# Kernel optimization log

Hardware: AMD Instinct MI355X
Metric: run time of the kernel (lower is better)

The kernel has to match this reference:

```python
import jax, jax.numpy as jnp
import numpy as np

H = 128
B, N = 8, 200
EPS = 1e-5


def _linear(v, W, b):
    return v @ W.T + b


def _masked_bn(v, m, gamma, beta):
    # v: (..., H); m: (...,) float 0/1 mask. BatchNorm1d over masked rows only
    # (track_running_stats=False -> batch statistics, biased variance).
    mf = m[..., None]
    axes = tuple(range(v.ndim - 1))
    cnt = jnp.maximum(jnp.sum(m), 1.0)
    mean = jnp.sum(v * mf, axis=axes) / cnt            # (H,)
    var = jnp.sum(mf * (v - mean) ** 2, axis=axes) / cnt
    vn = (v - mean) * jax.lax.rsqrt(var + EPS) * gamma + beta
    return jnp.where(mf > 0, vn, v)


def setup_inputs() -> dict:
    key = jax.random.key(0)
    ks = jax.random.split(key, 16)
    s = 1.0 / np.sqrt(H)
    p = lambda k, shp: jax.random.uniform(k, shp, jnp.float32, -s, s)
    return {
        "x": jax.random.normal(ks[0], (B, N, H), jnp.float32),
        "e": jax.random.normal(ks[1], (B, N, N, H), jnp.float32),
        "mask": jax.random.randint(ks[2], (B, N), 0, 2, jnp.int32),
        "Ue_W": p(ks[3], (H, H)), "Ue_b": p(ks[4], (H,)),
        "Ve_W": p(ks[5], (H, H)), "Ve_b": p(ks[6], (H,)),
        "Un_W": p(ks[7], (H, H)), "Un_b": p(ks[8], (H,)),
        "Vn_W": p(ks[9], (H, H)), "Vn_b": p(ks[10], (H,)),
        "bn_n_g": jnp.ones((H,), jnp.float32), "bn_n_b": jnp.zeros((H,), jnp.float32),
        "bn_e_g": jnp.ones((H,), jnp.float32), "bn_e_b": jnp.zeros((H,), jnp.float32),
    }


def reference(x, e, mask, Ue_W, Ue_b, Ve_W, Ve_b, Un_W, Un_b, Vn_W, Vn_b,
              bn_n_g, bn_n_b, bn_e_g, bn_e_b):
    m = mask.astype(x.dtype)                      # (B,N)
    m1 = m[..., None]                             # (B,N,1)
    sq_mask = m[:, :, None] * m[:, None, :]       # (B,N,N)

    # EdgeFeatures: e_ij = U*e_ij + V*x_i + V*x_j (with node-masked Vx)
    Vx = m1 * _linear(x, Ve_W, Ve_b)              # (B,N,H)
    e_tmp = _linear(e, Ue_W, Ue_b) + Vx[:, :, None, :] + Vx[:, None, :, :]

    gate = jax.nn.sigmoid(e_tmp)                  # (B,N,N,H)
    gate_m = gate * sq_mask[..., None]            # mask rows and cols

    # NodeFeatures, sum aggregation: x_i = U*x_i + sum_j gate_ij * (V*x_j)
    Ux = m1 * _linear(x, Un_W, Un_b)
    Vxn = m1 * _linear(x, Vn_W, Vn_b)
    agg = jnp.einsum("bijh,bjh->bih", gate_m, Vxn)
    x_tmp = Ux + agg

    e_bn = _masked_bn(e_tmp, sq_mask, bn_e_g, bn_e_b)
    x_bn = _masked_bn(x_tmp, m, bn_n_g, bn_n_b)

    x_new = x + jax.nn.relu(x_bn)
    e_new = e + jax.nn.relu(e_bn)
    return x_new, e_new
```

## Files before the change

kernel.cpp:

```cpp
#include <hip/hip_runtime.h>
#include <hip/hip_bf16.h>

namespace {

typedef __attribute__((ext_vector_type(8))) short short8;
typedef __attribute__((ext_vector_type(4))) float f32x4;

constexpr int H = 128;
constexpr int N = 200;
constexpr int BN = 1600;
constexpr int X_SIZE = BN * H;
constexpr int NH = N * H;
constexpr int NT = 13;

constexpr int WS_VX    = 0;
constexpr int WS_UX    = WS_VX + X_SIZE;
constexpr int WS_VXN   = WS_UX + X_SIZE;
constexpr int WS_XTMP  = WS_VXN + X_SIZE;
constexpr int WS_ESUMS = WS_XTMP + X_SIZE;
constexpr int WS_ESSQS = WS_ESUMS + 32 * H;
constexpr int WS_NSUMS = WS_ESSQS + 32 * H;
constexpr int WS_NSSQS = WS_NSUMS + 32 * H;
constexpr int WS_STAT_END = WS_NSSQS + 32 * H;
constexpr int WS_ESC   = WS_STAT_END;
constexpr int WS_ESH   = WS_ESC + H;
constexpr int WS_NSC   = WS_ESH + H;
constexpr int WS_NSH   = WS_NSC + H;

__device__ __forceinline__ unsigned short f2bf(float f) {
  __hip_bfloat16 h = __float2bfloat16(f);
  return __builtin_bit_cast(unsigned short, h);
}

__device__ __forceinline__ short8 pack8(f32x4 a, f32x4 b) {
  short8 r;
  r[0] = (short)f2bf(a[0]); r[1] = (short)f2bf(a[1]);
  r[2] = (short)f2bf(a[2]); r[3] = (short)f2bf(a[3]);
  r[4] = (short)f2bf(b[0]); r[5] = (short)f2bf(b[1]);
  r[6] = (short)f2bf(b[2]); r[7] = (short)f2bf(b[3]);
  return r;
}

__device__ __forceinline__ int xcd_bi(int bid) {
  return (bid & 7) * N + (bid >> 3);
}

__global__ __launch_bounds__(128) void k_prep(
    const float* __restrict__ x, const int* __restrict__ mask,
    const float* __restrict__ VeW, const float* __restrict__ Veb,
    const float* __restrict__ UnW, const float* __restrict__ Unb,
    const float* __restrict__ VnW, const float* __restrict__ Vnb,
    float* __restrict__ ws) {
  const int bi = blockIdx.x, h = threadIdx.x;
  __shared__ float xr[H];
  xr[h] = x[bi * H + h];
  __syncthreads();
  const float mi = (float)mask[bi];
  float a0 = 0.f, a1 = 0.f, a2 = 0.f;
  #pragma unroll 4
  for (int k = 0; k < H; k += 4) {
    const float x0 = xr[k], x1 = xr[k + 1], x2 = xr[k + 2], x3 = xr[k + 3];
    float4 w;
    w = *(const float4*)&VeW[h * H + k];
    a0 += w.x * x0 + w.y * x1 + w.z * x2 + w.w * x3;
    w = *(const float4*)&UnW[h * H + k];
    a1 += w.x * x0 + w.y * x1 + w.z * x2 + w.w * x3;
    w = *(const float4*)&VnW[h * H + k];
    a2 += w.x * x0 + w.y * x1 + w.z * x2 + w.w * x3;
  }
  ws[WS_VX  + bi * H + h] = mi * (a0 + Veb[h]);
  ws[WS_UX  + bi * H + h] = mi * (a1 + Unb[h]);
  ws[WS_VXN + bi * H + h] = mi * (a2 + Vnb[h]);
}

__global__ __launch_bounds__(256, 3) void k_edge0(
    const float* __restrict__ e, const int* __restrict__ mask,
    const float* __restrict__ UeW, const float* __restrict__ Ueb,
    float* __restrict__ ws) {
  const int bi = xcd_bi(blockIdx.x);
  const int b = bi / N;
  const int tid = threadIdx.x;
  const int w = tid >> 6, lane = tid & 63;
  const int l15 = lane & 15, lg = lane >> 4;
  const int hbase = w * 32;

  __shared__ float lds[2][3 * 2048];
  __shared__ float mrow[N];
  __shared__ float sS[H], sS2[H], sA[H];

  const float mi = (float)mask[bi];
  const float* __restrict__ eg  = e + (size_t)bi * NH;
  const float* __restrict__ vxg = ws + WS_VX  + (size_t)b * NH;
  const float* __restrict__ vng = ws + WS_VXN + (size_t)b * NH;

  auto stage = [&](int buf, int jt) {
    const int j0 = jt * 16;
    #pragma unroll
    for (int ii = 0; ii < 2; ++ii) {
      const int instr = 2 * w + ii;
      const int row = 2 * instr + (lane >> 5);
      const int gr = min(j0 + row, N - 1);
      const int sc16 = (lane & 31) ^ (row & 7);
      const size_t so = (size_t)gr * H + sc16 * 4;
      float* dst = &lds[buf][instr * 256];
      __builtin_amdgcn_global_load_lds(
          (const __attribute__((address_space(1))) void*)(eg + so),
          (__attribute__((address_space(3))) void*)dst, 16, 0, 0);
      __builtin_amdgcn_global_load_lds(
          (const __attribute__((address_space(1))) void*)(vxg + so),
          (__attribute__((address_space(3))) void*)(dst + 2048), 16, 0, 0);
      __builtin_amdgcn_global_load_lds(
          (const __attribute__((address_space(1))) void*)(vng + so),
          (__attribute__((address_space(3))) void*)(dst + 4096), 16, 0, 0);
    }
  };

  if (tid < N) mrow[tid] = (float)mask[b * N + tid];

  short8 Wf[2][4];
  #pragma unroll
  for (int ht = 0; ht < 2; ++ht) {
    const float* wr = &UeW[(size_t)(hbase + ht * 16 + l15) * H + lg * 8];
    #pragma unroll
    for (int s = 0; s < 4; ++s) {
      const f32x4 u0 = *(const f32x4*)(wr + s * 32);
      const f32x4 u1 = *(const f32x4*)(wr + s * 32 + 4);
      Wf[ht][s] = pack8(u0, u1);
    }
  }
  f32x4 base4[2];
  #pragma unroll
  for (int ht = 0; ht < 2; ++ht) {
    const int h0 = hbase + ht * 16 + 4 * lg;
    const f32x4 ub = *(const f32x4*)&Ueb[h0];
    const f32x4 vx = *(const f32x4*)&ws[WS_VX + (size_t)bi * H + h0];
    base4[ht] = ub + vx;
  }

  asm volatile("s_waitcnt vmcnt(0) lgkmcnt(0)" ::: "memory");
  __builtin_amdgcn_s_barrier();

  stage(0, 0);
  stage(1, 1);

  float bnS[2][4] = {{0,0,0,0},{0,0,0,0}};
  float bnS2[2][4] = {{0,0,0,0},{0,0,0,0}};
  float ag[2][4] = {{0,0,0,0},{0,0,0,0}};

  for (int jt = 0; jt < NT; ++jt) {
    if (jt < 12) asm volatile("s_waitcnt vmcnt(6)" ::: "memory");
    else         asm volatile("s_waitcnt vmcnt(0)" ::: "memory");
    __builtin_amdgcn_s_barrier();

    const float* tp = &lds[jt & 1][0];
    short8 Ef[4];
    #pragma unroll
    for (int s = 0; s < 4; ++s) {
      const int c0 = (lg * 2 + s * 8) ^ (l15 & 7);
      const int c1 = (lg * 2 + s * 8 + 1) ^ (l15 & 7);
      const f32x4 u0 = *(const f32x4*)&tp[l15 * 128 + c0 * 4];
      const f32x4 u1 = *(const f32x4*)&tp[l15 * 128 + c1 * 4];
      Ef[s] = pack8(u0, u1);
    }
    f32x4 vx4[2], vn4[2];
    #pragma unroll
    for (int ht = 0; ht < 2; ++ht) {
      const int h0 = hbase + ht * 16 + 4 * lg;
      const int ch = (h0 >> 2) ^ (l15 & 7);
      vx4[ht] = *(const f32x4*)&tp[2048 + l15 * 128 + ch * 4];
      vn4[ht] = *(const f32x4*)&tp[4096 + l15 * 128 + ch * 4];
    }

    asm volatile("s_waitcnt lgkmcnt(0)" ::: "memory");
    __builtin_amdgcn_sched_barrier(0);
    __builtin_amdgcn_s_barrier();

    if (jt + 2 < NT) stage(jt & 1, jt + 2);

    f32x4 acc[2] = {f32x4(0.f), f32x4(0.f)};
    #pragma unroll
    for (int s = 0; s < 4; ++s) {
      #pragma unroll
      for (int ht = 0; ht < 2; ++ht)
        acc[ht] = __builtin_amdgcn_mfma_f32_16x16x32_bf16(Wf[ht][s], Ef[s], acc[ht], 0, 0, 0);
    }

    const int j = jt * 16 + l15;
    const float msk = (j < N) ? mi * mrow[j < N ? j : 0] : 0.f;
    #pragma unroll
    for (int ht = 0; ht < 2; ++ht) {
      #pragma unroll
      for (int r = 0; r < 4; ++r) {
        const float v = acc[ht][r] + base4[ht][r] + vx4[ht][r];
        bnS[ht][r]  += msk * v;
        bnS2[ht][r] += msk * v * v;
        const float sg = __builtin_amdgcn_rcpf(1.f + __expf(-v));
        ag[ht][r] += msk * sg * vn4[ht][r];
      }
    }
  }

  #pragma unroll
  for (int ht = 0; ht < 2; ++ht) {
    #pragma unroll
    for (int r = 0; r < 4; ++r) {
      #pragma unroll
      for (int mm = 1; mm <= 8; mm <<= 1) {
        bnS[ht][r]  += __shfl_xor(bnS[ht][r], mm);
        bnS2[ht][r] += __shfl_xor(bnS2[ht][r], mm);
        ag[ht][r]   += __shfl_xor(ag[ht][r], mm);
      }
    }
  }
  if (l15 == 0) {
    #pragma unroll
    for (int ht = 0; ht < 2; ++ht) {
      #pragma unroll
      for (int r = 0; r < 4; ++r) {
        const int h = hbase + ht * 16 + 4 * lg + r;
        sS[h] = bnS[ht][r]; sS2[h] = bnS2[ht][r]; sA[h] = ag[ht][r];
      }
    }
  }
  __syncthreads();
  if (tid < H) {
    const int slot = (bi & 31) * H + tid;
    atomicAdd(&ws[WS_ESUMS + slot], sS[tid]);
    atomicAdd(&ws[WS_ESSQS + slot], sS2[tid]);
    const float v = ws[WS_UX + (size_t)bi * H + tid] + sA[tid];
    ws[WS_XTMP + (size_t)bi * H + tid] = v;
    atomicAdd(&ws[WS_NSUMS + slot], mi * v);
    atomicAdd(&ws[WS_NSSQS + slot], mi * v * v);
  }
}

__global__ void k_stats(const int* __restrict__ mask,
                        const float* __restrict__ beg, const float* __restrict__ beb,
                        const float* __restrict__ bng, const float* __restrict__ bnb,
                        float* __restrict__ ws) {
  __shared__ float sb[8];
  const int t = threadIdx.x;
  const int b = t >> 5, li = t & 31;
  float s = 0.f;
  for (int i = li; i < N; i += 32) s += (float)mask[b * N + i];
  #pragma unroll
  for (int o = 16; o >= 1; o >>= 1) s += __shfl_down(s, o, 32);
  if (li == 0) sb[b] = s;
  __syncthreads();
  if (t < H) {
    float cn = 0.f, ce = 0.f;
    #pragma unroll
    for (int bb = 0; bb < 8; ++bb) { cn += sb[bb]; ce += sb[bb] * sb[bb]; }
    ce = fmaxf(ce, 1.f); cn = fmaxf(cn, 1.f);
    float es = 0.f, es2 = 0.f, ns = 0.f, ns2 = 0.f;
    #pragma unroll 4
    for (int k = 0; k < 32; ++k) {
      es  += ws[WS_ESUMS + k * H + t];
      es2 += ws[WS_ESSQS + k * H + t];
      ns  += ws[WS_NSUMS + k * H + t];
      ns2 += ws[WS_NSSQS + k * H + t];
    }
    const float me = es / ce;
    const float ve = fmaxf(es2 / ce - me * me, 0.f);
    const float se = rsqrtf(ve + 1e-5f) * beg[t];
    ws[WS_ESC + t] = se;
    ws[WS_ESH + t] = beb[t] - me * se;
    const float mn = ns / cn;
    const float vn = fmaxf(ns2 / cn - mn * mn, 0.f);
    const float sn = rsqrtf(vn + 1e-5f) * bng[t];
    ws[WS_NSC + t] = sn;
    ws[WS_NSH + t] = bnb[t] - mn * sn;
  }
}

__global__ void k_x2(const float* __restrict__ x, const int* __restrict__ mask,
                     const float* __restrict__ ws, float* __restrict__ out) {
  const int idx = blockIdx.x * 256 + threadIdx.x;
  if (idx >= X_SIZE) return;
  const int h = idx & 127, bi = idx >> 7;
  const float v = ws[WS_XTMP + idx];
  const float r = (mask[bi] != 0) ? (v * ws[WS_NSC + h] + ws[WS_NSH + h]) : v;
  out[idx] = x[idx] + fmaxf(r, 0.f);
}

__global__ __launch_bounds__(256, 3) void k_edge1(
    const float* __restrict__ e, const int* __restrict__ mask,
    const float* __restrict__ UeW, const float* __restrict__ Ueb,
    const float* __restrict__ ws, float* __restrict__ out) {
  const int bi = xcd_bi(blockIdx.x);
  const int b = bi / N;
  const int tid = threadIdx.x;
  const int w = tid >> 6, lane = tid & 63;
  const int l15 = lane & 15, lg = lane >> 4;
  const int hbase = w * 32;

  __shared__ float lds[2][2 * 2048];
  __shared__ float mrow[N];

  const float mi = (float)mask[bi];
  const float* __restrict__ eg  = e + (size_t)bi * NH;
  const float* __restrict__ vxg = ws + WS_VX + (size_t)b * NH;

  auto stage = [&](int buf, int jt) {
    const int j0 = jt * 16;
    #pragma unroll
    for (int ii = 0; ii < 2; ++ii) {
      const int instr = 2 * w + ii;
      const int row = 2 * instr + (lane >> 5);
      const int gr = min(j0 + row, N - 1);
      const int sc16 = (lane & 31) ^ (row & 7);
      const size_t so = (size_t)gr * H + sc16 * 4;
      float* dst = &lds[buf][instr * 256];
      __builtin_amdgcn_global_load_lds(
          (const __attribute__((address_space(1))) void*)(eg + so),
          (__attribute__((address_space(3))) void*)dst, 16, 0, 0);
      __builtin_amdgcn_global_load_lds(
          (const __attribute__((address_space(1))) void*)(vxg + so),
          (__attribute__((address_space(3))) void*)(dst + 2048), 16, 0, 0);
    }
  };

  if (tid < N) mrow[tid] = (float)mask[b * N + tid];

  short8 Wf[2][4];
  #pragma unroll
  for (int ht = 0; ht < 2; ++ht) {
    const float* wr = &UeW[(size_t)(hbase + ht * 16 + l15) * H + lg * 8];
    #pragma unroll
    for (int s = 0; s < 4; ++s) {
      const f32x4 u0 = *(const f32x4*)(wr + s * 32);
      const f32x4 u1 = *(const f32x4*)(wr + s * 32 + 4);
      Wf[ht][s] = pack8(u0, u1);
    }
  }
  f32x4 base4[2], sc4[2], sh4[2];
  #pragma unroll
  for (int ht = 0; ht < 2; ++ht) {
    const int h0 = hbase + ht * 16 + 4 * lg;
    const f32x4 ub = *(const f32x4*)&Ueb[h0];
    const f32x4 vx = *(const f32x4*)&ws[WS_VX + (size_t)bi * H + h0];
    base4[ht] = ub + vx;
    sc4[ht] = *(const f32x4*)&ws[WS_ESC + h0];
    sh4[ht] = *(const f32x4*)&ws[WS_ESH + h0];
  }

  asm volatile("s_waitcnt vmcnt(0) lgkmcnt(0)" ::: "memory");
  __builtin_amdgcn_s_barrier();

  stage(0, 0);
  stage(1, 1);

  for (int jt = 0; jt < NT; ++jt) {
    if (jt == 0)      asm volatile("s_waitcnt vmcnt(4)" ::: "memory");
    else if (jt == 1) asm volatile("s_waitcnt vmcnt(6)" ::: "memory");
    else if (jt < 12) asm volatile("s_waitcnt vmcnt(8)" ::: "memory");
    else              asm volatile("s_waitcnt vmcnt(4)" ::: "memory");
    __builtin_amdgcn_s_barrier();

    const float* tp = &lds[jt & 1][0];
    short8 Ef[4];
    #pragma unroll
    for (int s = 0; s < 4; ++s) {
      const int c0 = (lg * 2 + s * 8) ^ (l15 & 7);
      const int c1 = (lg * 2 + s * 8 + 1) ^ (l15 & 7);
      const f32x4 u0 = *(const f32x4*)&tp[l15 * 128 + c0 * 4];
      const f32x4 u1 = *(const f32x4*)&tp[l15 * 128 + c1 * 4];
      Ef[s] = pack8(u0, u1);
    }
    f32x4 vx4[2], e4[2];
    #pragma unroll
    for (int ht = 0; ht < 2; ++ht) {
      const int h0 = hbase + ht * 16 + 4 * lg;
      const int ch = (h0 >> 2) ^ (l15 & 7);
      vx4[ht] = *(const f32x4*)&tp[2048 + l15 * 128 + ch * 4];
      e4[ht]  = *(const f32x4*)&tp[l15 * 128 + ch * 4];
    }

    asm volatile("s_waitcnt lgkmcnt(0)" ::: "memory");
    __builtin_amdgcn_sched_barrier(0);
    __builtin_amdgcn_s_barrier();

    if (jt + 2 < NT) stage(jt & 1, jt + 2);

    f32x4 acc[2] = {f32x4(0.f), f32x4(0.f)};
    #pragma unroll
    for (int s = 0; s < 4; ++s) {
      #pragma unroll
      for (int ht = 0; ht < 2; ++ht)
        acc[ht] = __builtin_amdgcn_mfma_f32_16x16x32_bf16(Wf[ht][s], Ef[s], acc[ht], 0, 0, 0);
    }

    const int j = jt * 16 + l15;
    if (j < N) {
      const float msk = mi * mrow[j];
      float* __restrict__ og = out + (size_t)X_SIZE + (size_t)bi * NH + (size_t)j * H;
      #pragma unroll
      for (int ht = 0; ht < 2; ++ht) {
        const int h0 = hbase + ht * 16 + 4 * lg;
        f32x4 o;
        #pragma unroll
        for (int r = 0; r < 4; ++r) {
          const float v = acc[ht][r] + base4[ht][r] + vx4[ht][r];
          const float rr = (msk > 0.f) ? (v * sc4[ht][r] + sh4[ht][r]) : v;
          o[r] = e4[ht][r] + fmaxf(rr, 0.f);
        }
        *(f32x4*)&og[h0] = o;
      }
    }
  }
}

}

extern "C" void kernel_launch(void* const* d_in, const int* in_sizes, int n_in,
                              void* d_out, int out_size, void* d_ws, size_t ws_size,
                              hipStream_t stream) {
  const float* x    = (const float*)d_in[0];
  const float* e    = (const float*)d_in[1];
  const int*   mask = (const int*)d_in[2];
  const float* UeW  = (const float*)d_in[3];
  const float* Ueb  = (const float*)d_in[4];
  const float* VeW  = (const float*)d_in[5];
  const float* Veb  = (const float*)d_in[6];
  const float* UnW  = (const float*)d_in[7];
  const float* Unb  = (const float*)d_in[8];
  const float* VnW  = (const float*)d_in[9];
  const float* Vnb  = (const float*)d_in[10];
  const float* bng  = (const float*)d_in[11];
  const float* bnb  = (const float*)d_in[12];
  const float* beg  = (const float*)d_in[13];
  const float* beb  = (const float*)d_in[14];
  float* ws  = (float*)d_ws;
  float* out = (float*)d_out;

  hipMemsetAsync(ws + WS_ESUMS, 0, (WS_STAT_END - WS_ESUMS) * sizeof(float), stream);
  k_prep<<<BN, 128, 0, stream>>>(x, mask, VeW, Veb, UnW, Unb, VnW, Vnb, ws);
  k_edge0<<<BN, 256, 0, stream>>>(e, mask, UeW, Ueb, ws);
  k_stats<<<1, 256, 0, stream>>>(mask, beg, beb, bng, bnb, ws);
  k_x2<<<800, 256, 0, stream>>>(x, mask, ws, out);
  k_edge1<<<BN, 256, 0, stream>>>(e, mask, UeW, Ueb, ws, out);
}
```

Before: 196.5 us.

## Split edge kernels over j-tiles across four blocks per row

Each (b,i) row of the edge kernels is now handled by four blocks, each covering a contiguous range of j tiles, so the grid has 6400 blocks instead of 1600. The node aggregate is accumulated with atomics into a new workspace buffer, and a new small kernel k_x1 forms x_tmp and the node batch-norm statistics afterwards. The XCD-aware block remap is dropped. This targets tail and wave-quantization effects and short per-block pipelines. In exchange it adds per-block weight loading overhead, shallower prefetch pipelines (3-4 tiles per block), an extra launch and more atomics.

```diff
diff --git a/kernel.cpp b/kernel.cpp
--- a/kernel.cpp
+++ b/kernel.cpp
@@ -12,12 +12,14 @@
 constexpr int X_SIZE = BN * H;
 constexpr int NH = N * H;
 constexpr int NT = 13;
+constexpr int JSPLIT = 4;
 
 constexpr int WS_VX    = 0;
 constexpr int WS_UX    = WS_VX + X_SIZE;
 constexpr int WS_VXN   = WS_UX + X_SIZE;
 constexpr int WS_XTMP  = WS_VXN + X_SIZE;
-constexpr int WS_ESUMS = WS_XTMP + X_SIZE;
+constexpr int WS_AGG   = WS_XTMP + X_SIZE;
+constexpr int WS_ESUMS = WS_AGG + X_SIZE;
 constexpr int WS_ESSQS = WS_ESUMS + 32 * H;
 constexpr int WS_NSUMS = WS_ESSQS + 32 * H;
 constexpr int WS_NSSQS = WS_NSUMS + 32 * H;
@@ -39,10 +41,6 @@
   r[4] = (short)f2bf(b[0]); r[5] = (short)f2bf(b[1]);
   r[6] = (short)f2bf(b[2]); r[7] = (short)f2bf(b[3]);
   return r;
-}
-
-__device__ __forceinline__ int xcd_bi(int bid) {
-  return (bid & 7) * N + (bid >> 3);
 }
 
 __global__ __launch_bounds__(128) void k_prep(
@@ -77,7 +75,10 @@
     const float* __restrict__ e, const int* __restrict__ mask,
     const float* __restrict__ UeW, const float* __restrict__ Ueb,
     float* __restrict__ ws) {
-  const int bi = xcd_bi(blockIdx.x);
+  const int bi = blockIdx.x >> 2;
+  const int c = blockIdx.x & 3;
+  const int jt0 = (NT * c) >> 2;
+  const int jt1 = (NT * (c + 1)) >> 2;
   const int b = bi / N;
   const int tid = threadIdx.x;
   const int w = tid >> 6, lane = tid & 63;
@@ -140,19 +141,19 @@
   asm volatile("s_waitcnt vmcnt(0) lgkmcnt(0)" ::: "memory");
   __builtin_amdgcn_s_barrier();
 
-  stage(0, 0);
-  stage(1, 1);
+  stage(0, jt0);
+  stage(1, jt0 + 1);
 
   float bnS[2][4] = {{0,0,0,0},{0,0,0,0}};
   float bnS2[2][4] = {{0,0,0,0},{0,0,0,0}};
   float ag[2][4] = {{0,0,0,0},{0,0,0,0}};
 
-  for (int jt = 0; jt < NT; ++jt) {
-    if (jt < 12) asm volatile("s_waitcnt vmcnt(6)" ::: "memory");
-    else         asm volatile("s_waitcnt vmcnt(0)" ::: "memory");
+  for (int jt = jt0; jt < jt1; ++jt) {
+    if (jt < jt1 - 1) asm volatile("s_waitcnt vmcnt(6)" ::: "memory");
+    else              asm volatile("s_waitcnt vmcnt(0)" ::: "memory");
     __builtin_amdgcn_s_barrier();
 
-    const float* tp = &lds[jt & 1][0];
+    const float* tp = &lds[(jt - jt0) & 1][0];
     short8 Ef[4];
     #pragma unroll
     for (int s = 0; s < 4; ++s) {
@@ -175,7 +176,7 @@
     __builtin_amdgcn_sched_barrier(0);
     __builtin_amdgcn_s_barrier();
 
-    if (jt + 2 < NT) stage(jt & 1, jt + 2);
+    if (jt + 2 < jt1) stage((jt - jt0) & 1, jt + 2);
 
     f32x4 acc[2] = {f32x4(0.f), f32x4(0.f)};
     #pragma unroll
@@ -224,14 +225,24 @@
   }
   __syncthreads();
   if (tid < H) {
-    const int slot = (bi & 31) * H + tid;
+    const int slot = ((int)blockIdx.x & 31) * H + tid;
     atomicAdd(&ws[WS_ESUMS + slot], sS[tid]);
     atomicAdd(&ws[WS_ESSQS + slot], sS2[tid]);
-    const float v = ws[WS_UX + (size_t)bi * H + tid] + sA[tid];
-    ws[WS_XTMP + (size_t)bi * H + tid] = v;
-    atomicAdd(&ws[WS_NSUMS + slot], mi * v);
-    atomicAdd(&ws[WS_NSSQS + slot], mi * v * v);
-  }
+    atomicAdd(&ws[WS_AGG + (size_t)bi * H + tid], sA[tid]);
+  }
+}
+
+__global__ void k_x1(const int* __restrict__ mask, float* __restrict__ ws) {
+  const int t = blockIdx.x * 256 + threadIdx.x;
+  const int h = t & 127, g = t >> 7;
+  float s = 0.f, s2 = 0.f;
+  for (int bi = g; bi < BN; bi += 100) {
+    const float v = ws[WS_UX + bi * H + h] + ws[WS_AGG + bi * H + h];
+    ws[WS_XTMP + bi * H + h] = v;
+    if (mask[bi] != 0) { s += v; s2 += v * v; }
+  }
+  atomicAdd(&ws[WS_NSUMS + (g & 31) * H + h], s);
+  atomicAdd(&ws[WS_NSSQS + (g & 31) * H + h], s2);
 }
 
 __global__ void k_stats(const int* __restrict__ mask,
@@ -287,7 +298,10 @@
     const float* __restrict__ e, const int* __restrict__ mask,
     const float* __restrict__ UeW, const float* __restrict__ Ueb,
     const float* __restrict__ ws, float* __restrict__ out) {
-  const int bi = xcd_bi(blockIdx.x);
+  const int bi = blockIdx.x >> 2;
+  const int c = blockIdx.x & 3;
+  const int jt0 = (NT * c) >> 2;
+  const int jt1 = (NT * (c + 1)) >> 2;
   const int b = bi / N;
   const int tid = threadIdx.x;
   const int w = tid >> 6, lane = tid & 63;
@@ -347,17 +361,17 @@
   asm volatile("s_waitcnt vmcnt(0) lgkmcnt(0)" ::: "memory");
   __builtin_amdgcn_s_barrier();
 
-  stage(0, 0);
-  stage(1, 1);
-
-  for (int jt = 0; jt < NT; ++jt) {
-    if (jt == 0)      asm volatile("s_waitcnt vmcnt(4)" ::: "memory");
-    else if (jt == 1) asm volatile("s_waitcnt vmcnt(6)" ::: "memory");
-    else if (jt < 12) asm volatile("s_waitcnt vmcnt(8)" ::: "memory");
-    else              asm volatile("s_waitcnt vmcnt(4)" ::: "memory");
+  stage(0, jt0);
+  stage(1, jt0 + 1);
+
+  for (int jt = jt0; jt < jt1; ++jt) {
+    if (jt == jt0)           asm volatile("s_waitcnt vmcnt(4)" ::: "memory");
+    else if (jt == jt1 - 1)  asm volatile("s_waitcnt vmcnt(4)" ::: "memory");
+    else if (jt == jt0 + 1)  asm volatile("s_waitcnt vmcnt(6)" ::: "memory");
+    else                     asm volatile("s_waitcnt vmcnt(8)" ::: "memory");
     __builtin_amdgcn_s_barrier();
 
-    const float* tp = &lds[jt & 1][0];
+    const float* tp = &lds[(jt - jt0) & 1][0];
     short8 Ef[4];
     #pragma unroll
     for (int s = 0; s < 4; ++s) {
@@ -380,7 +394,7 @@
     __builtin_amdgcn_sched_barrier(0);
     __builtin_amdgcn_s_barrier();
 
-    if (jt + 2 < NT) stage(jt & 1, jt + 2);
+    if (jt + 2 < jt1) stage((jt - jt0) & 1, jt + 2);
 
     f32x4 acc[2] = {f32x4(0.f), f32x4(0.f)};
     #pragma unroll
@@ -433,10 +447,11 @@
   float* ws  = (float*)d_ws;
   float* out = (float*)d_out;
 
-  hipMemsetAsync(ws + WS_ESUMS, 0, (WS_STAT_END - WS_ESUMS) * sizeof(float), stream);
+  hipMemsetAsync(ws + WS_AGG, 0, (WS_STAT_END - WS_AGG) * sizeof(float), stream);
   k_prep<<<BN, 128, 0, stream>>>(x, mask, VeW, Veb, UnW, Unb, VnW, Vnb, ws);
-  k_edge0<<<BN, 256, 0, stream>>>(e, mask, UeW, Ueb, ws);
+  k_edge0<<<BN * JSPLIT, 256, 0, stream>>>(e, mask, UeW, Ueb, ws);
+  k_x1<<<50, 256, 0, stream>>>(mask, ws);
   k_stats<<<1, 256, 0, stream>>>(mask, beg, beb, bng, bnb, ws);
   k_x2<<<800, 256, 0, stream>>>(x, mask, ws, out);
-  k_edge1<<<BN, 256, 0, stream>>>(e, mask, UeW, Ueb, ws, out);
-}
+  k_edge1<<<BN * JSPLIT, 256, 0, stream>>>(e, mask, UeW, Ueb, ws, out);
+}
```

Measured after the change: 268.0 us. +36.4%, slower.

## Load Vx/Vxn rows directly to registers instead of staging through LDS

Applied to the files above, without the earlier changes.

The edge kernels no longer stage the per-j Vx and Vxn rows through LDS with global_load_lds. Each lane now reads just the slices it needs with direct global vector loads, and only e is double-buffered in LDS. The smaller LDS footprint allows raising the occupancy hint from 3 to 4 blocks per CU. The XCD-aware block remapping is removed and blocks now map linearly to rows. The risks are global load latency inside the loop, which is no longer hidden by the prefetch pipeline, and possibly worse L2 locality for the shared Vx rows without the XCD swizzle.

```diff
diff --git a/kernel.cpp b/kernel.cpp
--- a/kernel.cpp
+++ b/kernel.cpp
@@ -39,10 +39,6 @@
   r[4] = (short)f2bf(b[0]); r[5] = (short)f2bf(b[1]);
   r[6] = (short)f2bf(b[2]); r[7] = (short)f2bf(b[3]);
   return r;
-}
-
-__device__ __forceinline__ int xcd_bi(int bid) {
-  return (bid & 7) * N + (bid >> 3);
 }
 
 __global__ __launch_bounds__(128) void k_prep(
@@ -73,25 +69,27 @@
   ws[WS_VXN + bi * H + h] = mi * (a2 + Vnb[h]);
 }
 
-__global__ __launch_bounds__(256, 3) void k_edge0(
+__global__ __launch_bounds__(256, 4) void k_edge0(
     const float* __restrict__ e, const int* __restrict__ mask,
     const float* __restrict__ UeW, const float* __restrict__ Ueb,
     float* __restrict__ ws) {
-  const int bi = xcd_bi(blockIdx.x);
+  const int bi = blockIdx.x;
   const int b = bi / N;
   const int tid = threadIdx.x;
   const int w = tid >> 6, lane = tid & 63;
   const int l15 = lane & 15, lg = lane >> 4;
   const int hbase = w * 32;
-
-  __shared__ float lds[2][3 * 2048];
+  const int h0a = hbase + 4 * lg;
+  const int h0b = hbase + 16 + 4 * lg;
+
+  __shared__ float lds[2][2048];
   __shared__ float mrow[N];
   __shared__ float sS[H], sS2[H], sA[H];
 
   const float mi = (float)mask[bi];
   const float* __restrict__ eg  = e + (size_t)bi * NH;
-  const float* __restrict__ vxg = ws + WS_VX  + (size_t)b * NH;
-  const float* __restrict__ vng = ws + WS_VXN + (size_t)b * NH;
+  const float* __restrict__ vxb = ws + WS_VX  + (size_t)b * NH;
+  const float* __restrict__ vnb = ws + WS_VXN + (size_t)b * NH;
 
   auto stage = [&](int buf, int jt) {
     const int j0 = jt * 16;
@@ -106,12 +104,6 @@
       __builtin_amdgcn_global_load_lds(
           (const __attribute__((address_space(1))) void*)(eg + so),
           (__attribute__((address_space(3))) void*)dst, 16, 0, 0);
-      __builtin_amdgcn_global_load_lds(
-          (const __attribute__((address_space(1))) void*)(vxg + so),
-          (__attribute__((address_space(3))) void*)(dst + 2048), 16, 0, 0);
-      __builtin_amdgcn_global_load_lds(
-          (const __attribute__((address_space(1))) void*)(vng + so),
-          (__attribute__((address_space(3))) void*)(dst + 4096), 16, 0, 0);
     }
   };
 
@@ -148,9 +140,15 @@
   float ag[2][4] = {{0,0,0,0},{0,0,0,0}};
 
   for (int jt = 0; jt < NT; ++jt) {
-    if (jt < 12) asm volatile("s_waitcnt vmcnt(6)" ::: "memory");
+    if (jt < 12) asm volatile("s_waitcnt vmcnt(2)" ::: "memory");
     else         asm volatile("s_waitcnt vmcnt(0)" ::: "memory");
     __builtin_amdgcn_s_barrier();
+
+    const size_t ro = (size_t)min(jt * 16 + l15, N - 1) * H;
+    const f32x4 gx0 = *(const f32x4*)&vxb[ro + h0a];
+    const f32x4 gx1 = *(const f32x4*)&vxb[ro + h0b];
+    const f32x4 gn0 = *(const f32x4*)&vnb[ro + h0a];
+    const f32x4 gn1 = *(const f32x4*)&vnb[ro + h0b];
 
     const float* tp = &lds[jt & 1][0];
     short8 Ef[4];
@@ -162,14 +160,6 @@
       const f32x4 u1 = *(const f32x4*)&tp[l15 * 128 + c1 * 4];
       Ef[s] = pack8(u0, u1);
     }
-    f32x4 vx4[2], vn4[2];
-    #pragma unroll
-    for (int ht = 0; ht < 2; ++ht) {
-      const int h0 = hbase + ht * 16 + 4 * lg;
-      const int ch = (h0 >> 2) ^ (l15 & 7);
-      vx4[ht] = *(const f32x4*)&tp[2048 + l15 * 128 + ch * 4];
-      vn4[ht] = *(const f32x4*)&tp[4096 + l15 * 128 + ch * 4];
-    }
 
     asm volatile("s_waitcnt lgkmcnt(0)" ::: "memory");
     __builtin_amdgcn_sched_barrier(0);
@@ -188,15 +178,15 @@
     const int j = jt * 16 + l15;
     const float msk = (j < N) ? mi * mrow[j < N ? j : 0] : 0.f;
     #pragma unroll
-    for (int ht = 0; ht < 2; ++ht) {
-      #pragma unroll
-      for (int r = 0; r < 4; ++r) {
-        const float v = acc[ht][r] + base4[ht][r] + vx4[ht][r];
-        bnS[ht][r]  += msk * v;
-        bnS2[ht][r] += msk * v * v;
-        const float sg = __builtin_amdgcn_rcpf(1.f + __expf(-v));
-        ag[ht][r] += msk * sg * vn4[ht][r];
-      }
+    for (int r = 0; r < 4; ++r) {
+      const float v0 = acc[0][r] + base4[0][r] + gx0[r];
+      bnS[0][r]  += msk * v0;
+      bnS2[0][r] += msk * v0 * v0;
+      ag[0][r]   += msk * __builtin_amdgcn_rcpf(1.f + __expf(-v0)) * gn0[r];
+      const float v1 = acc[1][r] + base4[1][r] + gx1[r];
+      bnS[1][r]  += msk * v1;
+      bnS2[1][r] += msk * v1 * v1;
+      ag[1][r]   += msk * __builtin_amdgcn_rcpf(1.f + __expf(-v1)) * gn1[r];
     }
   }
 
@@ -283,23 +273,25 @@
   out[idx] = x[idx] + fmaxf(r, 0.f);
 }
 
-__global__ __launch_bounds__(256, 3) void k_edge1(
+__global__ __launch_bounds__(256, 4) void k_edge1(
     const float* __restrict__ e, const int* __restrict__ mask,
     const float* __restrict__ UeW, const float* __restrict__ Ueb,
     const float* __restrict__ ws, float* __restrict__ out) {
-  const int bi = xcd_bi(blockIdx.x);
+  const int bi = blockIdx.x;
   const int b = bi / N;
   const int tid = threadIdx.x;
   const int w = tid >> 6, lane = tid & 63;
   const int l15 = lane & 15, lg = lane >> 4;
   const int hbase = w * 32;
-
-  __shared__ float lds[2][2 * 2048];
+  const int h0a = hbase + 4 * lg;
+  const int h0b = hbase + 16 + 4 * lg;
+
+  __shared__ float lds[2][2048];
   __shared__ float mrow[N];
 
   const float mi = (float)mask[bi];
   const float* __restrict__ eg  = e + (size_t)bi * NH;
-  const float* __restrict__ vxg = ws + WS_VX + (size_t)b * NH;
+  const float* __restrict__ vxb = ws + WS_VX + (size_t)b * NH;
 
   auto stage = [&](int buf, int jt) {
     const int j0 = jt * 16;
@@ -314,9 +306,6 @@
       __builtin_amdgcn_global_load_lds(
           (const __attribute__((address_space(1))) void*)(eg + so),
           (__attribute__((address_space(3))) void*)dst, 16, 0, 0);
-      __builtin_amdgcn_global_load_lds(
-          (const __attribute__((address_space(1))) void*)(vxg + so),
-          (__attribute__((address_space(3))) void*)(dst + 2048), 16, 0, 0);
     }
   };
 
@@ -351,11 +340,13 @@
   stage(1, 1);
 
   for (int jt = 0; jt < NT; ++jt) {
-    if (jt == 0)      asm volatile("s_waitcnt vmcnt(4)" ::: "memory");
-    else if (jt == 1) asm volatile("s_waitcnt vmcnt(6)" ::: "memory");
-    else if (jt < 12) asm volatile("s_waitcnt vmcnt(8)" ::: "memory");
-    else              asm volatile("s_waitcnt vmcnt(4)" ::: "memory");
+    if (jt < 12) asm volatile("s_waitcnt vmcnt(2)" ::: "memory");
+    else         asm volatile("s_waitcnt vmcnt(0)" ::: "memory");
     __builtin_amdgcn_s_barrier();
+
+    const size_t ro = (size_t)min(jt * 16 + l15, N - 1) * H;
+    const f32x4 gx0 = *(const f32x4*)&vxb[ro + h0a];
+    const f32x4 gx1 = *(const f32x4*)&vxb[ro + h0b];
 
     const float* tp = &lds[jt & 1][0];
     short8 Ef[4];
@@ -367,13 +358,12 @@
       const f32x4 u1 = *(const f32x4*)&tp[l15 * 128 + c1 * 4];
       Ef[s] = pack8(u0, u1);
     }
-    f32x4 vx4[2], e4[2];
+    f32x4 e4[2];
     #pragma unroll
     for (int ht = 0; ht < 2; ++ht) {
       const int h0 = hbase + ht * 16 + 4 * lg;
       const int ch = (h0 >> 2) ^ (l15 & 7);
-      vx4[ht] = *(const f32x4*)&tp[2048 + l15 * 128 + ch * 4];
-      e4[ht]  = *(const f32x4*)&tp[l15 * 128 + ch * 4];
+      e4[ht] = *(const f32x4*)&tp[l15 * 128 + ch * 4];
     }
 
     asm volatile("s_waitcnt lgkmcnt(0)" ::: "memory");
@@ -394,18 +384,18 @@
     if (j < N) {
       const float msk = mi * mrow[j];
       float* __restrict__ og = out + (size_t)X_SIZE + (size_t)bi * NH + (size_t)j * H;
+      f32x4 o0, o1;
       #pragma unroll
-      for (int ht = 0; ht < 2; ++ht) {
-        const int h0 = hbase + ht * 16 + 4 * lg;
-        f32x4 o;
-        #pragma unroll
-        for (int r = 0; r < 4; ++r) {
-          const float v = acc[ht][r] + base4[ht][r] + vx4[ht][r];
-          const float rr = (msk > 0.f) ? (v * sc4[ht][r] + sh4[ht][r]) : v;
-          o[r] = e4[ht][r] + fmaxf(rr, 0.f);
-        }
-        *(f32x4*)&og[h0] = o;
+      for (int r = 0; r < 4; ++r) {
+        const float v0 = acc[0][r] + base4[0][r] + gx0[r];
+        const float r0 = (msk > 0.f) ? (v0 * sc4[0][r] + sh4[0][r]) : v0;
+        o0[r] = e4[0][r] + fmaxf(r0, 0.f);
+        const float v1 = acc[1][r] + base4[1][r] + gx1[r];
+        const float r1 = (msk > 0.f) ? (v1 * sc4[1][r] + sh4[1][r]) : v1;
+        o1[r] = e4[1][r] + fmaxf(r1, 0.f);
       }
+      *(f32x4*)&og[h0a] = o0;
+      *(f32x4*)&og[h0b] = o1;
     }
   }
 }
```

Measured after the change: 275.6 us. 40.2% more time.
